# Kernel optimization log

Measured on AMD Instinct MI355X. Metric: run time of the kernel, lower is better.

## Reference

```python
import jax, jax.numpy as jnp
import numpy as np

DEPTH = 2
DIM = 64
INNER = 256  # hard-coded inner_dim in Attention
HEADS = 1
N = 4096
B = 2
EPS = 1e-5


def layernorm(x, g, b):
    m = jnp.mean(x, axis=-1, keepdims=True)
    v = jnp.var(x, axis=-1, keepdims=True)
    return (x - m) * jax.lax.rsqrt(v + EPS) * g + b


def setup_inputs() -> dict:
    key = jax.random.key(0)
    ks = jax.random.split(key, 16)
    embed = jax.random.normal(ks[0], (B, N, DIM), dtype=jnp.float32)
    A = jax.random.randint(ks[1], (1, HEADS, N, N), 0, 2).astype(jnp.float32)
    s = 0.02
    return {
        "embed": embed,
        "A": A,
        "g1": jnp.ones((DEPTH, DIM), jnp.float32),
        "b1": jnp.zeros((DEPTH, DIM), jnp.float32),
        "Wqkv": jax.random.normal(ks[2], (DEPTH, DIM, INNER * 3), jnp.float32) * s,
        "Wout": jax.random.normal(ks[3], (DEPTH, INNER, DIM), jnp.float32) * s,
        "bout": jnp.zeros((DEPTH, DIM), jnp.float32),
        "g2": jnp.ones((DEPTH, DIM), jnp.float32),
        "b2": jnp.zeros((DEPTH, DIM), jnp.float32),
        "W1": jax.random.normal(ks[4], (DEPTH, DIM, DIM), jnp.float32) * s,
        "bb1": jnp.zeros((DEPTH, DIM), jnp.float32),
        "W2": jax.random.normal(ks[5], (DEPTH, DIM, DIM), jnp.float32) * s,
        "bb2": jnp.zeros((DEPTH, DIM), jnp.float32),
        "gf": jnp.ones((DIM,), jnp.float32),
        "bf": jnp.zeros((DIM,), jnp.float32),
    }


def _encoder(embed, A, g1, b1, Wqkv, Wout, bout, g2, b2, W1, bb1, W2, bb2, gf, bf):
    b, n, dim = embed.shape
    scale = dim ** (-0.5)
    dh = INNER // HEADS
    x = embed
    attn = None
    dots_softmax = None
    diag = jnp.arange(n)
    for l in range(DEPTH):
        xn = layernorm(x, g1[l], b1[l])
        qkv = xn @ Wqkv[l]  # [b, n, 3*INNER]
        q, k, v = jnp.split(qkv, 3, axis=-1)
        # [b, n, INNER] -> [b, h, n, dh]
        q = q.reshape(b, n, HEADS, dh).transpose(0, 2, 1, 3)
        k = k.reshape(b, n, HEADS, dh).transpose(0, 2, 1, 3)
        v = v.reshape(b, n, HEADS, dh).transpose(0, 2, 1, 3)
        dots = jnp.einsum("bhid,bhjd->bhij", q, k) * scale
        dots_softmax = jax.nn.softmax(dots[0, 0], axis=-1)
        # adjacency mask, then only [0][0] kept; diagonal filled with literal 1.0;
        # the original does a cpu/numpy roundtrip with .detach() -> stop_gradient.
        e = jnp.where(A > 0, dots, jnp.float32(-9e15))[0, 0]  # [n, n]
        e = e.at[diag, diag].set(1.0)
        e = jax.lax.stop_gradient(e)
        attn = jax.nn.softmax(e, axis=-1)  # [n, n], shared across b, h
        out = jnp.einsum("ij,bhjd->bhid", attn, v)  # broadcast attn over b,h
        out = out.transpose(0, 2, 1, 3).reshape(b, n, INNER)
        out = out @ Wout[l] + bout[l]
        x = xn + out  # residual onto the NORMED input (as in original)
        xm = layernorm(x, g2[l], b2[l])
        mlp = jax.nn.gelu(xm @ W1[l] + bb1[l], approximate=False) @ W2[l] + bb2[l]
        x = xm + mlp
    x = layernorm(x, gf, bf)
    return x, attn.reshape(1, 1, n, n), dots_softmax


def reference(embed, A, g1, b1, Wqkv, Wout, bout, g2, b2, W1, bb1, W2, bb2, gf, bf):
    return _encoder(embed, A, g1, b1, Wqkv, Wout, bout, g2, b2, W1, bb1, W2, bb2, gf, bf)
```

## Files before the change

### kernel.cpp

```cpp
#include <hip/hip_runtime.h>
#include <hip/hip_bf16.h>
#include <math.h>

typedef __attribute__((ext_vector_type(8))) short short8;
typedef __attribute__((ext_vector_type(4))) float f32x4;

__device__ __forceinline__ unsigned short f2bf(float x) {
    __hip_bfloat16 b = __float2bfloat16(x);
    return *reinterpret_cast<unsigned short*>(&b);
}
__device__ __forceinline__ float gelu_exact(float x) {
    return 0.5f * x * (1.0f + erff(x * 0.70710678118654752f));
}

__global__ __launch_bounds__(256) void k_zero(float* __restrict__ p, long n)
{
    long i = (long)blockIdx.x * 256 + threadIdx.x;
    if (i < n) p[i] = 0.f;
}

__global__ __launch_bounds__(256) void k_layernorm(
    const float* __restrict__ x, const float* __restrict__ g,
    const float* __restrict__ b, float* __restrict__ out)
{
    int wave = threadIdx.x >> 6, lane = threadIdx.x & 63;
    long row = (long)blockIdx.x * 4 + wave;
    float v = x[row * 64 + lane];
    float s = v;
    #pragma unroll
    for (int o = 32; o; o >>= 1) s += __shfl_xor(s, o);
    float m = s * (1.0f / 64.0f);
    float d = v - m;
    float q = d * d;
    #pragma unroll
    for (int o = 32; o; o >>= 1) q += __shfl_xor(q, o);
    float rstd = rsqrtf(q * (1.0f / 64.0f) + 1e-5f);
    out[row * 64 + lane] = d * rstd * g[lane] + b[lane];
}

__global__ __launch_bounds__(256) void k_wfold(
    const float* __restrict__ Wqkv, const float* __restrict__ Wout,
    float* __restrict__ Wfold)
{
    int idx = blockIdx.x * 256 + threadIdx.x;
    int c = idx >> 6, d = idx & 63;
    float a = 0.f;
    for (int k = 0; k < 256; ++k)
        a += Wqkv[c * 768 + 512 + k] * Wout[k * 64 + d];
    Wfold[idx] = a;
}

__global__ __launch_bounds__(256) void k_maskpack(
    const float* __restrict__ Aadj, unsigned long long* __restrict__ mask)
{
    int row = blockIdx.x;
    int wave = threadIdx.x >> 6, lane = threadIdx.x & 63;
    for (int w = wave; w < 64; w += 4) {
        float a = Aadj[(long)row * 4096 + w * 64 + lane];
        unsigned long long m = __ballot(a > 0.f);
        if (lane == 0) mask[(long)row * 64 + w] = m;
    }
}

__global__ __launch_bounds__(256) void k_qk(
    const float* __restrict__ xn, const float* __restrict__ W,
    unsigned short* __restrict__ q, unsigned short* __restrict__ kmat)
{
    __shared__ float As[64][65];
    __shared__ float Ws[64][65];
    int tid = threadIdx.x;
    int m0 = blockIdx.x * 64, n0 = blockIdx.y * 64;
    #pragma unroll
    for (int it = 0; it < 16; ++it) {
        int idx = tid + it * 256;
        int r = idx >> 6, c = idx & 63;
        As[r][c] = xn[(long)(m0 + r) * 64 + c];
        Ws[r][c] = W[(long)r * 768 + n0 + c];
    }
    __syncthreads();
    int tx = tid & 15, ty = tid >> 4;
    float acc[4][4] = {};
    #pragma unroll
    for (int k = 0; k < 64; ++k) {
        float a[4], w[4];
        #pragma unroll
        for (int i = 0; i < 4; ++i) a[i] = As[ty * 4 + i][k];
        #pragma unroll
        for (int j = 0; j < 4; ++j) w[j] = Ws[k][tx * 4 + j];
        #pragma unroll
        for (int i = 0; i < 4; ++i)
            #pragma unroll
            for (int j = 0; j < 4; ++j) acc[i][j] += a[i] * w[j];
    }
    #pragma unroll
    for (int i = 0; i < 4; ++i) {
        long row = m0 + ty * 4 + i;
        #pragma unroll
        for (int j = 0; j < 4; ++j) {
            int col = n0 + tx * 4 + j;
            if (col < 256) q[row * 256 + col] = f2bf(acc[i][j]);
            else           kmat[row * 256 + (col - 256)] = f2bf(acc[i][j]);
        }
    }
}

__global__ __launch_bounds__(256) void k_xnw_t(
    const float* __restrict__ xn, const float* __restrict__ Wfold,
    unsigned short* __restrict__ vWT)
{
    __shared__ float As[64][65];
    __shared__ float Ws[64][65];
    int tid = threadIdx.x;
    int n0 = blockIdx.x * 64, b = blockIdx.y;
    #pragma unroll
    for (int it = 0; it < 16; ++it) {
        int idx = tid + it * 256;
        int r = idx >> 6, c = idx & 63;
        As[r][c] = xn[((long)b * 4096 + n0 + r) * 64 + c];
        Ws[r][c] = Wfold[r * 64 + c];
    }
    __syncthreads();
    int tx = tid & 15, ty = tid >> 4;
    float acc[4][4] = {};
    #pragma unroll
    for (int k = 0; k < 64; ++k) {
        float a[4], w[4];
        #pragma unroll
        for (int i = 0; i < 4; ++i) a[i] = As[ty * 4 + i][k];
        #pragma unroll
        for (int j = 0; j < 4; ++j) w[j] = Ws[k][tx * 4 + j];
        #pragma unroll
        for (int i = 0; i < 4; ++i)
            #pragma unroll
            for (int j = 0; j < 4; ++j) acc[i][j] += a[i] * w[j];
    }
    #pragma unroll
    for (int i = 0; i < 4; ++i)
        #pragma unroll
        for (int j = 0; j < 4; ++j)
            vWT[((long)b * 64 + tx * 4 + j) * 4096 + n0 + ty * 4 + i] = f2bf(acc[i][j]);
}

__global__ __launch_bounds__(256) void k_mfma_nt(
    const unsigned short* __restrict__ A, const unsigned short* __restrict__ B,
    float* __restrict__ C, int N, int K, float scale)
{
    __shared__ __align__(16) unsigned short As[128 * 64];
    __shared__ __align__(16) unsigned short Bs[128 * 64];
    int tid = threadIdx.x;
    int lane = tid & 63, wave = tid >> 6;
    long m0 = (long)blockIdx.x * 128, n0 = (long)blockIdx.y * 128;
    const unsigned short* Ag = A + m0 * K;
    const unsigned short* Bg = B + n0 * K;
    int wm = (wave & 1) * 64, wn = (wave >> 1) * 64;
    int fr = lane & 15, quad = lane >> 4;

    f32x4 acc[4][4];
    #pragma unroll
    for (int i = 0; i < 4; ++i)
        #pragma unroll
        for (int j = 0; j < 4; ++j) acc[i][j] = (f32x4){0.f, 0.f, 0.f, 0.f};

    for (int k0 = 0; k0 < K; k0 += 64) {
        #pragma unroll
        for (int it = 0; it < 4; ++it) {
            int c = tid + it * 256;
            int r = c >> 3, col = (c & 7) * 8;
            *(short8*)&As[c * 8] = *(const short8*)(Ag + (long)r * K + k0 + col);
            *(short8*)&Bs[c * 8] = *(const short8*)(Bg + (long)r * K + k0 + col);
        }
        __syncthreads();
        #pragma unroll
        for (int ks = 0; ks < 2; ++ks) {
            short8 af[4], bfr[4];
            #pragma unroll
            for (int i = 0; i < 4; ++i) {
                af[i]  = *(const short8*)&As[(wm + i * 16 + fr) * 64 + ks * 32 + quad * 8];
                bfr[i] = *(const short8*)&Bs[(wn + i * 16 + fr) * 64 + ks * 32 + quad * 8];
            }
            #pragma unroll
            for (int i = 0; i < 4; ++i)
                #pragma unroll
                for (int j = 0; j < 4; ++j)
                    acc[i][j] = __builtin_amdgcn_mfma_f32_16x16x32_bf16(
                        af[i], bfr[j], acc[i][j], 0, 0, 0);
        }
        __syncthreads();
    }
    #pragma unroll
    for (int i = 0; i < 4; ++i) {
        #pragma unroll
        for (int j = 0; j < 4; ++j) {
            long col = n0 + wn + j * 16 + fr;
            long rowb = m0 + wm + i * 16 + quad * 4;
            #pragma unroll
            for (int r = 0; r < 4; ++r)
                C[(rowb + r) * N + col] = acc[i][j][r] * scale;
        }
    }
}

__global__ __launch_bounds__(256) void k_mfma_splitk(
    const float* __restrict__ A, const unsigned short* __restrict__ B,
    float* __restrict__ C)
{
    __shared__ __align__(16) unsigned short As[128 * 64];
    __shared__ __align__(16) unsigned short Bs[128 * 64];
    const int K = 4096, N = 128;
    int tid = threadIdx.x;
    int lane = tid & 63, wave = tid >> 6;
    long m0 = (long)blockIdx.x * 128;
    int k0base = blockIdx.y * 512;
    const float* Ag = A + m0 * K;
    int wm = (wave & 1) * 64, wn = (wave >> 1) * 64;
    int fr = lane & 15, quad = lane >> 4;

    f32x4 acc[4][4];
    #pragma unroll
    for (int i = 0; i < 4; ++i)
        #pragma unroll
        for (int j = 0; j < 4; ++j) acc[i][j] = (f32x4){0.f, 0.f, 0.f, 0.f};

    for (int k0 = k0base; k0 < k0base + 512; k0 += 64) {
        #pragma unroll
        for (int it = 0; it < 4; ++it) {
            int c = tid + it * 256;
            int r = c >> 3, col = (c & 7) * 8;
            float4 f0 = *(const float4*)(Ag + (long)r * K + k0 + col);
            float4 f1 = *(const float4*)(Ag + (long)r * K + k0 + col + 4);
            short8 s;
            s[0] = (short)f2bf(f0.x); s[1] = (short)f2bf(f0.y);
            s[2] = (short)f2bf(f0.z); s[3] = (short)f2bf(f0.w);
            s[4] = (short)f2bf(f1.x); s[5] = (short)f2bf(f1.y);
            s[6] = (short)f2bf(f1.z); s[7] = (short)f2bf(f1.w);
            *(short8*)&As[c * 8] = s;
            *(short8*)&Bs[c * 8] = *(const short8*)(B + (long)r * K + k0 + col);
        }
        __syncthreads();
        #pragma unroll
        for (int ks = 0; ks < 2; ++ks) {
            short8 af[4], bfr[4];
            #pragma unroll
            for (int i = 0; i < 4; ++i) {
                af[i]  = *(const short8*)&As[(wm + i * 16 + fr) * 64 + ks * 32 + quad * 8];
                bfr[i] = *(const short8*)&Bs[(wn + i * 16 + fr) * 64 + ks * 32 + quad * 8];
            }
            #pragma unroll
            for (int i = 0; i < 4; ++i)
                #pragma unroll
                for (int j = 0; j < 4; ++j)
                    acc[i][j] = __builtin_amdgcn_mfma_f32_16x16x32_bf16(
                        af[i], bfr[j], acc[i][j], 0, 0, 0);
        }
        __syncthreads();
    }
    #pragma unroll
    for (int i = 0; i < 4; ++i) {
        #pragma unroll
        for (int j = 0; j < 4; ++j) {
            long col = wn + j * 16 + fr;
            long rowb = m0 + wm + i * 16 + quad * 4;
            #pragma unroll
            for (int r = 0; r < 4; ++r)
                atomicAdd(&C[(rowb + r) * N + col], acc[i][j][r]);
        }
    }
}

__device__ __forceinline__ float block_max(float v, float* red, int lane, int wave) {
    #pragma unroll
    for (int o = 32; o; o >>= 1) v = fmaxf(v, __shfl_xor(v, o));
    if (lane == 0) red[wave] = v;
    __syncthreads();
    v = fmaxf(fmaxf(red[0], red[1]), fmaxf(red[2], red[3]));
    __syncthreads();
    return v;
}
__device__ __forceinline__ float block_sum(float v, float* red, int lane, int wave) {
    #pragma unroll
    for (int o = 32; o; o >>= 1) v += __shfl_xor(v, o);
    if (lane == 0) red[wave] = v;
    __syncthreads();
    v = red[0] + red[1] + red[2] + red[3];
    __syncthreads();
    return v;
}

__global__ __launch_bounds__(256) void k_softmax_attn(
    float* __restrict__ dots, const float* __restrict__ Aadj,
    const unsigned long long* __restrict__ mask,
    float* __restrict__ attn_out, int write_ds)
{
    __shared__ float red[4];
    __shared__ unsigned long long msk[64];
    int row = blockIdx.x, tid = threadIdx.x;
    int lane = tid & 63, wave = tid >> 6;
    float* drow = dots + (long)row * 4096;
    if (mask) {
        if (tid < 64) msk[tid] = mask[(long)row * 64 + tid];
        __syncthreads();
    }
    float d[16], mv[16];
    float mmax = -1e30f, umax = -1e30f;
    #pragma unroll
    for (int i = 0; i < 16; ++i) {
        int j = tid + i * 256;
        float dv = drow[j];
        d[i] = dv;
        bool keep = mask ? ((msk[j >> 6] >> (j & 63)) & 1ull)
                         : (Aadj[(long)row * 4096 + j] > 0.f);
        float m = keep ? dv : -1e30f;
        if (j == row) m = 1.0f;
        mv[i] = m;
        mmax = fmaxf(mmax, m);
        umax = fmaxf(umax, dv);
    }
    float M1 = block_max(mmax, red, lane, wave);
    float s1 = 0.f;
    #pragma unroll
    for (int i = 0; i < 16; ++i) { float e = expf(mv[i] - M1); mv[i] = e; s1 += e; }
    s1 = block_sum(s1, red, lane, wave);
    float inv1 = 1.0f / s1;
    #pragma unroll
    for (int i = 0; i < 16; ++i)
        attn_out[(long)row * 4096 + tid + i * 256] = mv[i] * inv1;

    if (write_ds) {
        float M2 = block_max(umax, red, lane, wave);
        float s2 = 0.f;
        #pragma unroll
        for (int i = 0; i < 16; ++i) { float e = expf(d[i] - M2); d[i] = e; s2 += e; }
        s2 = block_sum(s2, red, lane, wave);
        float inv2 = 1.0f / s2;
        #pragma unroll
        for (int i = 0; i < 16; ++i)
            drow[tid + i * 256] = d[i] * inv2;
    }
}

__global__ __launch_bounds__(256) void k_avres(
    const float* __restrict__ xn, const float* __restrict__ avcat,
    const float* __restrict__ bout, float* __restrict__ x)
{
    int idx = blockIdx.x * 256 + threadIdx.x;
    int r = idx >> 6, c = idx & 63;
    int b = r >> 12, n = r & 4095;
    x[idx] = xn[idx] + avcat[(long)n * 128 + b * 64 + c] + bout[c];
}

__global__ __launch_bounds__(256) void k_gemm64(
    const float* __restrict__ A, const float* __restrict__ W,
    const float* __restrict__ bias, const float* __restrict__ res,
    float* __restrict__ out, int act)
{
    __shared__ float As[64][65];
    __shared__ float Ws[64][65];
    int tid = threadIdx.x;
    int m0 = blockIdx.x * 64;
    #pragma unroll
    for (int it = 0; it < 16; ++it) {
        int idx = tid + it * 256;
        int r = idx >> 6, c = idx & 63;
        As[r][c] = A[(long)(m0 + r) * 64 + c];
        Ws[r][c] = W[(long)r * 64 + c];
    }
    __syncthreads();
    int tx = tid & 15, ty = tid >> 4;
    float acc[4][4] = {};
    #pragma unroll
    for (int k = 0; k < 64; ++k) {
        float a[4], w[4];
        #pragma unroll
        for (int i = 0; i < 4; ++i) a[i] = As[ty * 4 + i][k];
        #pragma unroll
        for (int j = 0; j < 4; ++j) w[j] = Ws[k][tx * 4 + j];
        #pragma unroll
        for (int i = 0; i < 4; ++i)
            #pragma unroll
            for (int j = 0; j < 4; ++j) acc[i][j] += a[i] * w[j];
    }
    #pragma unroll
    for (int i = 0; i < 4; ++i) {
        long row = m0 + ty * 4 + i;
        #pragma unroll
        for (int j = 0; j < 4; ++j) {
            int col = tx * 4 + j;
            float v = acc[i][j] + bias[col];
            if (act) v = gelu_exact(v);
            if (res) v += res[row * 64 + col];
            out[row * 64 + col] = v;
        }
    }
}

extern "C" void kernel_launch(void* const* d_in, const int* in_sizes, int n_in,
                              void* d_out, int out_size, void* d_ws, size_t ws_size,
                              hipStream_t stream)
{
    const float* embed = (const float*)d_in[0];
    const float* Aadj  = (const float*)d_in[1];
    const float* g1    = (const float*)d_in[2];
    const float* b1    = (const float*)d_in[3];
    const float* Wqkv  = (const float*)d_in[4];
    const float* Wout  = (const float*)d_in[5];
    const float* bout  = (const float*)d_in[6];
    const float* g2    = (const float*)d_in[7];
    const float* b2    = (const float*)d_in[8];
    const float* W1    = (const float*)d_in[9];
    const float* bb1   = (const float*)d_in[10];
    const float* W2    = (const float*)d_in[11];
    const float* bb2   = (const float*)d_in[12];
    const float* gf    = (const float*)d_in[13];
    const float* bff   = (const float*)d_in[14];

    float* ox    = (float*)d_out;
    float* attnb = ox + 524288;
    float* dsb   = attnb + 16777216;

    if (ws_size < (10ull << 20)) {
        k_zero<<<133120, 256, 0, stream>>>(ox, 34078720l);
        return;
    }

    char* ws = (char*)d_ws;
    float*          x     = (float*)(ws + (0l << 20));
    float*          xn    = (float*)(ws + (2l << 20));
    float*          h     = (float*)(ws + (4l << 20));
    unsigned short* q     = (unsigned short*)(ws + (6l << 20));
    unsigned short* kmat  = (unsigned short*)(ws + (7l << 20));
    unsigned short* vwt   = (unsigned short*)(ws + (8l << 20));
    float*          Wfold = (float*)(ws + (9l << 20));
    unsigned long long* mask = (ws_size >= (12ull << 20))
        ? (unsigned long long*)(ws + (10l << 20)) : nullptr;

    if (mask) k_maskpack<<<4096, 256, 0, stream>>>(Aadj, mask);

    for (int l = 0; l < 2; ++l) {
        const float* Wq = Wqkv + (long)l * 64 * 768;
        k_layernorm<<<2048, 256, 0, stream>>>(l ? x : embed, g1 + 64 * l, b1 + 64 * l, xn);
        k_wfold<<<16, 256, 0, stream>>>(Wq, Wout + (long)l * 256 * 64, Wfold);
        k_qk<<<dim3(64, 8), 256, 0, stream>>>(xn, Wq, q, kmat);
        k_xnw_t<<<dim3(64, 2), 256, 0, stream>>>(xn, Wfold, vwt);
        k_mfma_nt<<<dim3(32, 32), 256, 0, stream>>>(q, kmat, dsb, 4096, 256, 0.125f);
        k_softmax_attn<<<4096, 256, 0, stream>>>(dsb, Aadj, mask, attnb, l == 1);
        k_zero<<<2048, 256, 0, stream>>>(ox, 524288l);
        k_mfma_splitk<<<dim3(32, 8), 256, 0, stream>>>(attnb, vwt, ox);
        k_avres<<<2048, 256, 0, stream>>>(xn, ox, bout + 64 * l, x);
        k_layernorm<<<2048, 256, 0, stream>>>(x, g2 + 64 * l, b2 + 64 * l, xn);
        k_gemm64<<<128, 256, 0, stream>>>(xn, W1 + (long)l * 4096, bb1 + 64 * l,
                                          nullptr, h, 1);
        k_gemm64<<<128, 256, 0, stream>>>(h, W2 + (long)l * 4096, bb2 + 64 * l,
                                          xn, x, 0);
    }
    k_layernorm<<<2048, 256, 0, stream>>>(x, gf, bff, ox);
}
```

Measured before the change: 520.3 us.

## Fuse tail MLP/layernorms, store dots and attn in bf16, batch weight folding

Several changes are combined. The residual, layernorm, both MLP GEMMs and the next or final layernorm are fused into one tail kernel. The Q/K and V-fold projections merge into one launch, and both layers' Wfold and the mask are built up front. When workspace allows, the dots and attention matrices are kept in bf16 scratch, and the fp32 attention and softmax outputs are written only for the final layer. This cuts launches and the large fp32 N×N traffic, at the cost of more bf16 rounding in layer 0's scores and branchy code paths that depend on workspace size.

New measurement: 536.4 us. 3.1% more time.

```diff
diff --git a/kernel.cpp b/kernel.cpp
--- a/kernel.cpp
+++ b/kernel.cpp
@@ -8,6 +8,9 @@
 __device__ __forceinline__ unsigned short f2bf(float x) {
     __hip_bfloat16 b = __float2bfloat16(x);
     return *reinterpret_cast<unsigned short*>(&b);
+}
+__device__ __forceinline__ float bfu2f(unsigned short u) {
+    union { unsigned u; float f; } c; c.u = ((unsigned)u) << 16; return c.f;
 }
 __device__ __forceinline__ float gelu_exact(float x) {
     return 0.5f * x * (1.0f + erff(x * 0.70710678118654752f));
@@ -38,15 +41,18 @@
     out[row * 64 + lane] = d * rstd * g[lane] + b[lane];
 }
 
-__global__ __launch_bounds__(256) void k_wfold(
+__global__ __launch_bounds__(256) void k_wfold2(
     const float* __restrict__ Wqkv, const float* __restrict__ Wout,
     float* __restrict__ Wfold)
 {
     int idx = blockIdx.x * 256 + threadIdx.x;
-    int c = idx >> 6, d = idx & 63;
+    int l = idx >> 12, rem = idx & 4095;
+    int c = rem >> 6, d = rem & 63;
+    const float* Wq = Wqkv + (long)l * 49152;
+    const float* Wo = Wout + (long)l * 16384;
     float a = 0.f;
     for (int k = 0; k < 256; ++k)
-        a += Wqkv[c * 768 + 512 + k] * Wout[k * 64 + d];
+        a += Wq[c * 768 + 512 + k] * Wo[k * 64 + d];
     Wfold[idx] = a;
 }
 
@@ -62,20 +68,26 @@
     }
 }
 
-__global__ __launch_bounds__(256) void k_qk(
+__global__ __launch_bounds__(256) void k_qkxnw(
     const float* __restrict__ xn, const float* __restrict__ W,
-    unsigned short* __restrict__ q, unsigned short* __restrict__ kmat)
+    const float* __restrict__ Wfold,
+    unsigned short* __restrict__ q, unsigned short* __restrict__ kmat,
+    unsigned short* __restrict__ vwt)
 {
     __shared__ float As[64][65];
     __shared__ float Ws[64][65];
     int tid = threadIdx.x;
-    int m0 = blockIdx.x * 64, n0 = blockIdx.y * 64;
+    int y = blockIdx.y;
+    int qk = (y < 8);
+    int m0, b = 0, n0;
+    if (qk) { m0 = blockIdx.x * 64; n0 = y * 64; }
+    else    { b = y - 8; m0 = b * 4096 + blockIdx.x * 64; n0 = 0; }
     #pragma unroll
     for (int it = 0; it < 16; ++it) {
         int idx = tid + it * 256;
         int r = idx >> 6, c = idx & 63;
         As[r][c] = xn[(long)(m0 + r) * 64 + c];
-        Ws[r][c] = W[(long)r * 768 + n0 + c];
+        Ws[r][c] = qk ? W[(long)r * 768 + n0 + c] : Wfold[r * 64 + c];
     }
     __syncthreads();
     int tx = tid & 15, ty = tid >> 4;
@@ -92,61 +104,34 @@
             #pragma unroll
             for (int j = 0; j < 4; ++j) acc[i][j] += a[i] * w[j];
     }
-    #pragma unroll
-    for (int i = 0; i < 4; ++i) {
-        long row = m0 + ty * 4 + i;
-        #pragma unroll
-        for (int j = 0; j < 4; ++j) {
-            int col = n0 + tx * 4 + j;
-            if (col < 256) q[row * 256 + col] = f2bf(acc[i][j]);
-            else           kmat[row * 256 + (col - 256)] = f2bf(acc[i][j]);
-        }
-    }
-}
-
-__global__ __launch_bounds__(256) void k_xnw_t(
-    const float* __restrict__ xn, const float* __restrict__ Wfold,
-    unsigned short* __restrict__ vWT)
-{
-    __shared__ float As[64][65];
-    __shared__ float Ws[64][65];
-    int tid = threadIdx.x;
-    int n0 = blockIdx.x * 64, b = blockIdx.y;
-    #pragma unroll
-    for (int it = 0; it < 16; ++it) {
-        int idx = tid + it * 256;
-        int r = idx >> 6, c = idx & 63;
-        As[r][c] = xn[((long)b * 4096 + n0 + r) * 64 + c];
-        Ws[r][c] = Wfold[r * 64 + c];
-    }
-    __syncthreads();
-    int tx = tid & 15, ty = tid >> 4;
-    float acc[4][4] = {};
-    #pragma unroll
-    for (int k = 0; k < 64; ++k) {
-        float a[4], w[4];
-        #pragma unroll
-        for (int i = 0; i < 4; ++i) a[i] = As[ty * 4 + i][k];
-        #pragma unroll
-        for (int j = 0; j < 4; ++j) w[j] = Ws[k][tx * 4 + j];
+    if (qk) {
+        #pragma unroll
+        for (int i = 0; i < 4; ++i) {
+            long row = m0 + ty * 4 + i;
+            #pragma unroll
+            for (int j = 0; j < 4; ++j) {
+                int col = n0 + tx * 4 + j;
+                if (col < 256) q[row * 256 + col] = f2bf(acc[i][j]);
+                else           kmat[row * 256 + (col - 256)] = f2bf(acc[i][j]);
+            }
+        }
+    } else {
+        int nb = blockIdx.x * 64;
         #pragma unroll
         for (int i = 0; i < 4; ++i)
             #pragma unroll
-            for (int j = 0; j < 4; ++j) acc[i][j] += a[i] * w[j];
-    }
-    #pragma unroll
-    for (int i = 0; i < 4; ++i)
-        #pragma unroll
-        for (int j = 0; j < 4; ++j)
-            vWT[((long)b * 64 + tx * 4 + j) * 4096 + n0 + ty * 4 + i] = f2bf(acc[i][j]);
-}
-
-__global__ __launch_bounds__(256) void k_mfma_nt(
+            for (int j = 0; j < 4; ++j)
+                vwt[((long)b * 64 + tx * 4 + j) * 4096 + nb + ty * 4 + i] = f2bf(acc[i][j]);
+    }
+}
+
+__global__ __launch_bounds__(256) void k_dots(
     const unsigned short* __restrict__ A, const unsigned short* __restrict__ B,
-    float* __restrict__ C, int N, int K, float scale)
+    unsigned short* __restrict__ Ch, float* __restrict__ Cf)
 {
     __shared__ __align__(16) unsigned short As[128 * 64];
     __shared__ __align__(16) unsigned short Bs[128 * 64];
+    const int K = 256;
     int tid = threadIdx.x;
     int lane = tid & 63, wave = tid >> 6;
     long m0 = (long)blockIdx.x * 128, n0 = (long)blockIdx.y * 128;
@@ -194,15 +179,18 @@
             long col = n0 + wn + j * 16 + fr;
             long rowb = m0 + wm + i * 16 + quad * 4;
             #pragma unroll
-            for (int r = 0; r < 4; ++r)
-                C[(rowb + r) * N + col] = acc[i][j][r] * scale;
-        }
-    }
-}
-
-__global__ __launch_bounds__(256) void k_mfma_splitk(
-    const float* __restrict__ A, const unsigned short* __restrict__ B,
-    float* __restrict__ C)
+            for (int r = 0; r < 4; ++r) {
+                float v = acc[i][j][r] * 0.125f;
+                if (Ch) Ch[(rowb + r) * 4096 + col] = f2bf(v);
+                else    Cf[(rowb + r) * 4096 + col] = v;
+            }
+        }
+    }
+}
+
+__global__ __launch_bounds__(256) void k_splitk(
+    const unsigned short* __restrict__ Ah, const float* __restrict__ Af,
+    const unsigned short* __restrict__ B, float* __restrict__ C)
 {
     __shared__ __align__(16) unsigned short As[128 * 64];
     __shared__ __align__(16) unsigned short Bs[128 * 64];
@@ -211,7 +199,6 @@
     int lane = tid & 63, wave = tid >> 6;
     long m0 = (long)blockIdx.x * 128;
     int k0base = blockIdx.y * 512;
-    const float* Ag = A + m0 * K;
     int wm = (wave & 1) * 64, wn = (wave >> 1) * 64;
     int fr = lane & 15, quad = lane >> 4;
 
@@ -226,14 +213,20 @@
         for (int it = 0; it < 4; ++it) {
             int c = tid + it * 256;
             int r = c >> 3, col = (c & 7) * 8;
-            float4 f0 = *(const float4*)(Ag + (long)r * K + k0 + col);
-            float4 f1 = *(const float4*)(Ag + (long)r * K + k0 + col + 4);
-            short8 s;
-            s[0] = (short)f2bf(f0.x); s[1] = (short)f2bf(f0.y);
-            s[2] = (short)f2bf(f0.z); s[3] = (short)f2bf(f0.w);
-            s[4] = (short)f2bf(f1.x); s[5] = (short)f2bf(f1.y);
-            s[6] = (short)f2bf(f1.z); s[7] = (short)f2bf(f1.w);
-            *(short8*)&As[c * 8] = s;
+            if (Ah) {
+                *(short8*)&As[c * 8] =
+                    *(const short8*)(Ah + (m0 + r) * (long)K + k0 + col);
+            } else {
+                const float* Ag = Af + m0 * K;
+                float4 f0 = *(const float4*)(Ag + (long)r * K + k0 + col);
+                float4 f1 = *(const float4*)(Ag + (long)r * K + k0 + col + 4);
+                short8 s;
+                s[0] = (short)f2bf(f0.x); s[1] = (short)f2bf(f0.y);
+                s[2] = (short)f2bf(f0.z); s[3] = (short)f2bf(f0.w);
+                s[4] = (short)f2bf(f1.x); s[5] = (short)f2bf(f1.y);
+                s[6] = (short)f2bf(f1.z); s[7] = (short)f2bf(f1.w);
+                *(short8*)&As[c * 8] = s;
+            }
             *(short8*)&Bs[c * 8] = *(const short8*)(B + (long)r * K + k0 + col);
         }
         __syncthreads();
@@ -286,31 +279,28 @@
     return v;
 }
 
-__global__ __launch_bounds__(256) void k_softmax_attn(
-    float* __restrict__ dots, const float* __restrict__ Aadj,
-    const unsigned long long* __restrict__ mask,
-    float* __restrict__ attn_out, int write_ds)
+__global__ __launch_bounds__(256) void k_softmax_bf(
+    const unsigned short* __restrict__ dots, const unsigned long long* __restrict__ mask,
+    unsigned short* __restrict__ attn_h, float* __restrict__ attn_f,
+    float* __restrict__ ds)
 {
     __shared__ float red[4];
-    __shared__ unsigned long long msk[64];
     int row = blockIdx.x, tid = threadIdx.x;
     int lane = tid & 63, wave = tid >> 6;
-    float* drow = dots + (long)row * 4096;
-    if (mask) {
-        if (tid < 64) msk[tid] = mask[(long)row * 64 + tid];
-        __syncthreads();
-    }
+    long base = (long)row * 4096 + tid * 16;
+    short8 v0 = *(const short8*)(dots + base);
+    short8 v1 = *(const short8*)(dots + base + 8);
+    unsigned long long mw = mask[(long)row * 64 + (tid >> 2)];
+    int mbase = (tid & 3) * 16;
+    int idiag = row - tid * 16;
     float d[16], mv[16];
     float mmax = -1e30f, umax = -1e30f;
     #pragma unroll
     for (int i = 0; i < 16; ++i) {
-        int j = tid + i * 256;
-        float dv = drow[j];
+        float dv = bfu2f((unsigned short)(i < 8 ? v0[i] : v1[i - 8]));
         d[i] = dv;
-        bool keep = mask ? ((msk[j >> 6] >> (j & 63)) & 1ull)
-                         : (Aadj[(long)row * 4096 + j] > 0.f);
-        float m = keep ? dv : -1e30f;
-        if (j == row) m = 1.0f;
+        float m = ((mw >> (mbase + i)) & 1ull) ? dv : -1e30f;
+        if (i == idiag) m = 1.0f;
         mv[i] = m;
         mmax = fmaxf(mmax, m);
         umax = fmaxf(umax, dv);
@@ -321,11 +311,22 @@
     for (int i = 0; i < 16; ++i) { float e = expf(mv[i] - M1); mv[i] = e; s1 += e; }
     s1 = block_sum(s1, red, lane, wave);
     float inv1 = 1.0f / s1;
-    #pragma unroll
-    for (int i = 0; i < 16; ++i)
-        attn_out[(long)row * 4096 + tid + i * 256] = mv[i] * inv1;
-
-    if (write_ds) {
+    short8 o0, o1;
+    #pragma unroll
+    for (int i = 0; i < 16; ++i) {
+        float p = mv[i] * inv1;
+        mv[i] = p;
+        if (i < 8) o0[i] = (short)f2bf(p); else o1[i - 8] = (short)f2bf(p);
+    }
+    *(short8*)(attn_h + base) = o0;
+    *(short8*)(attn_h + base + 8) = o1;
+    if (attn_f) {
+        #pragma unroll
+        for (int i = 0; i < 4; ++i)
+            *(float4*)(attn_f + base + i * 4) =
+                (float4){mv[i * 4], mv[i * 4 + 1], mv[i * 4 + 2], mv[i * 4 + 3]};
+    }
+    if (ds) {
         float M2 = block_max(umax, red, lane, wave);
         float s2 = 0.f;
         #pragma unroll
@@ -333,63 +334,172 @@
         s2 = block_sum(s2, red, lane, wave);
         float inv2 = 1.0f / s2;
         #pragma unroll
-        for (int i = 0; i < 16; ++i)
-            drow[tid + i * 256] = d[i] * inv2;
-    }
-}
-
-__global__ __launch_bounds__(256) void k_avres(
+        for (int i = 0; i < 4; ++i)
+            *(float4*)(ds + base + i * 4) =
+                (float4){d[i * 4] * inv2, d[i * 4 + 1] * inv2,
+                         d[i * 4 + 2] * inv2, d[i * 4 + 3] * inv2};
+    }
+}
+
+__global__ __launch_bounds__(256) void k_softmax_f32(
+    float* __restrict__ dots, const unsigned long long* __restrict__ mask,
+    float* __restrict__ attn_f)
+{
+    __shared__ float red[4];
+    int row = blockIdx.x, tid = threadIdx.x;
+    int lane = tid & 63, wave = tid >> 6;
+    long base = (long)row * 4096 + tid * 16;
+    float d[16], mv[16];
+    #pragma unroll
+    for (int i = 0; i < 4; ++i) {
+        float4 f = *(const float4*)(dots + base + i * 4);
+        d[i * 4] = f.x; d[i * 4 + 1] = f.y; d[i * 4 + 2] = f.z; d[i * 4 + 3] = f.w;
+    }
+    unsigned long long mw = mask[(long)row * 64 + (tid >> 2)];
+    int mbase = (tid & 3) * 16;
+    int idiag = row - tid * 16;
+    float mmax = -1e30f, umax = -1e30f;
+    #pragma unroll
+    for (int i = 0; i < 16; ++i) {
+        float m = ((mw >> (mbase + i)) & 1ull) ? d[i] : -1e30f;
+        if (i == idiag) m = 1.0f;
+        mv[i] = m;
+        mmax = fmaxf(mmax, m);
+        umax = fmaxf(umax, d[i]);
+    }
+    float M1 = block_max(mmax, red, lane, wave);
+    float s1 = 0.f;
+    #pragma unroll
+    for (int i = 0; i < 16; ++i) { float e = expf(mv[i] - M1); mv[i] = e; s1 += e; }
+    s1 = block_sum(s1, red, lane, wave);
+    float inv1 = 1.0f / s1;
+    #pragma unroll
+    for (int i = 0; i < 4; ++i)
+        *(float4*)(attn_f + base + i * 4) =
+            (float4){mv[i * 4] * inv1, mv[i * 4 + 1] * inv1,
+                     mv[i * 4 + 2] * inv1, mv[i * 4 + 3] * inv1};
+    float M2 = block_max(umax, red, lane, wave);
+    float s2 = 0.f;
+    #pragma unroll
+    for (int i = 0; i < 16; ++i) { float e = expf(d[i] - M2); d[i] = e; s2 += e; }
+    s2 = block_sum(s2, red, lane, wave);
+    float inv2 = 1.0f / s2;
+    #pragma unroll
+    for (int i = 0; i < 4; ++i)
+        *(float4*)(dots + base + i * 4) =
+            (float4){d[i * 4] * inv2, d[i * 4 + 1] * inv2,
+                     d[i * 4 + 2] * inv2, d[i * 4 + 3] * inv2};
+}
+
+__global__ __launch_bounds__(256) void k_tail(
     const float* __restrict__ xn, const float* __restrict__ avcat,
-    const float* __restrict__ bout, float* __restrict__ x)
-{
-    int idx = blockIdx.x * 256 + threadIdx.x;
-    int r = idx >> 6, c = idx & 63;
-    int b = r >> 12, n = r & 4095;
-    x[idx] = xn[idx] + avcat[(long)n * 128 + b * 64 + c] + bout[c];
-}
-
-__global__ __launch_bounds__(256) void k_gemm64(
-    const float* __restrict__ A, const float* __restrict__ W,
-    const float* __restrict__ bias, const float* __restrict__ res,
-    float* __restrict__ out, int act)
-{
-    __shared__ float As[64][65];
-    __shared__ float Ws[64][65];
+    const float* __restrict__ bout,
+    const float* __restrict__ g2, const float* __restrict__ b2,
+    const float* __restrict__ W1, const float* __restrict__ bb1,
+    const float* __restrict__ W2, const float* __restrict__ bb2,
+    const float* __restrict__ gn, const float* __restrict__ bn,
+    float* __restrict__ out)
+{
+    __shared__ float X[64][65], XM[64][65], H[64][65], WS[64][65];
     int tid = threadIdx.x;
     int m0 = blockIdx.x * 64;
+    int wv = tid >> 6, ln = tid & 63;
     #pragma unroll
     for (int it = 0; it < 16; ++it) {
         int idx = tid + it * 256;
         int r = idx >> 6, c = idx & 63;
-        As[r][c] = A[(long)(m0 + r) * 64 + c];
-        Ws[r][c] = W[(long)r * 64 + c];
+        int gr = m0 + r;
+        X[r][c] = xn[(long)gr * 64 + c]
+                + avcat[(long)(gr & 4095) * 128 + (gr >> 12) * 64 + c]
+                + bout[c];
+    }
+    __syncthreads();
+    #pragma unroll
+    for (int rr = 0; rr < 16; ++rr) {
+        int r = wv * 16 + rr;
+        float v = X[r][ln];
+        float s = v;
+        #pragma unroll
+        for (int o = 32; o; o >>= 1) s += __shfl_xor(s, o);
+        float m = s * (1.0f / 64.0f);
+        float dd = v - m;
+        float q = dd * dd;
+        #pragma unroll
+        for (int o = 32; o; o >>= 1) q += __shfl_xor(q, o);
+        float rstd = rsqrtf(q * (1.0f / 64.0f) + 1e-5f);
+        XM[r][ln] = dd * rstd * g2[ln] + b2[ln];
+    }
+    __syncthreads();
+    #pragma unroll
+    for (int it = 0; it < 16; ++it) {
+        int idx = tid + it * 256;
+        WS[idx >> 6][idx & 63] = W1[idx];
     }
     __syncthreads();
     int tx = tid & 15, ty = tid >> 4;
-    float acc[4][4] = {};
-    #pragma unroll
-    for (int k = 0; k < 64; ++k) {
-        float a[4], w[4];
-        #pragma unroll
-        for (int i = 0; i < 4; ++i) a[i] = As[ty * 4 + i][k];
-        #pragma unroll
-        for (int j = 0; j < 4; ++j) w[j] = Ws[k][tx * 4 + j];
+    {
+        float acc[4][4] = {};
+        #pragma unroll
+        for (int k = 0; k < 64; ++k) {
+            float a[4], w[4];
+            #pragma unroll
+            for (int i = 0; i < 4; ++i) a[i] = XM[ty * 4 + i][k];
+            #pragma unroll
+            for (int j = 0; j < 4; ++j) w[j] = WS[k][tx * 4 + j];
+            #pragma unroll
+            for (int i = 0; i < 4; ++i)
+                #pragma unroll
+                for (int j = 0; j < 4; ++j) acc[i][j] += a[i] * w[j];
+        }
         #pragma unroll
         for (int i = 0; i < 4; ++i)
             #pragma unroll
-            for (int j = 0; j < 4; ++j) acc[i][j] += a[i] * w[j];
-    }
-    #pragma unroll
-    for (int i = 0; i < 4; ++i) {
-        long row = m0 + ty * 4 + i;
-        #pragma unroll
-        for (int j = 0; j < 4; ++j) {
-            int col = tx * 4 + j;
-            float v = acc[i][j] + bias[col];
-            if (act) v = gelu_exact(v);
-            if (res) v += res[row * 64 + col];
-            out[row * 64 + col] = v;
-        }
+            for (int j = 0; j < 4; ++j)
+                H[ty * 4 + i][tx * 4 + j] = gelu_exact(acc[i][j] + bb1[tx * 4 + j]);
+    }
+    __syncthreads();
+    #pragma unroll
+    for (int it = 0; it < 16; ++it) {
+        int idx = tid + it * 256;
+        WS[idx >> 6][idx & 63] = W2[idx];
+    }
+    __syncthreads();
+    {
+        float acc[4][4] = {};
+        #pragma unroll
+        for (int k = 0; k < 64; ++k) {
+            float a[4], w[4];
+            #pragma unroll
+            for (int i = 0; i < 4; ++i) a[i] = H[ty * 4 + i][k];
+            #pragma unroll
+            for (int j = 0; j < 4; ++j) w[j] = WS[k][tx * 4 + j];
+            #pragma unroll
+            for (int i = 0; i < 4; ++i)
+                #pragma unroll
+                for (int j = 0; j < 4; ++j) acc[i][j] += a[i] * w[j];
+        }
+        #pragma unroll
+        for (int i = 0; i < 4; ++i)
+            #pragma unroll
+            for (int j = 0; j < 4; ++j)
+                X[ty * 4 + i][tx * 4 + j] =
+                    XM[ty * 4 + i][tx * 4 + j] + acc[i][j] + bb2[tx * 4 + j];
+    }
+    __syncthreads();
+    #pragma unroll
+    for (int rr = 0; rr < 16; ++rr) {
+        int r = wv * 16 + rr;
+        float v = X[r][ln];
+        float s = v;
+        #pragma unroll
+        for (int o = 32; o; o >>= 1) s += __shfl_xor(s, o);
+        float m = s * (1.0f / 64.0f);
+        float dd = v - m;
+        float q = dd * dd;
+        #pragma unroll
+        for (int o = 32; o; o >>= 1) q += __shfl_xor(q, o);
+        float rstd = rsqrtf(q * (1.0f / 64.0f) + 1e-5f);
+        out[(long)(m0 + r) * 64 + ln] = dd * rstd * gn[ln] + bn[ln];
     }
 }
 
@@ -423,34 +533,49 @@
     }
 
     char* ws = (char*)d_ws;
-    float*          x     = (float*)(ws + (0l << 20));
-    float*          xn    = (float*)(ws + (2l << 20));
-    float*          h     = (float*)(ws + (4l << 20));
-    unsigned short* q     = (unsigned short*)(ws + (6l << 20));
-    unsigned short* kmat  = (unsigned short*)(ws + (7l << 20));
-    unsigned short* vwt   = (unsigned short*)(ws + (8l << 20));
-    float*          Wfold = (float*)(ws + (9l << 20));
-    unsigned long long* mask = (ws_size >= (12ull << 20))
-        ? (unsigned long long*)(ws + (10l << 20)) : nullptr;
-
-    if (mask) k_maskpack<<<4096, 256, 0, stream>>>(Aadj, mask);
+    float*          xn    = (float*)(ws + (0l << 20));
+    float*          avcat = (float*)(ws + (2l << 20));
+    unsigned short* q     = (unsigned short*)(ws + (4l << 20));
+    unsigned short* kmat  = (unsigned short*)(ws + (5l << 20));
+    unsigned short* vwt   = (unsigned short*)(ws + (6l << 20));
+    float*          Wfold = (float*)(ws + (7l << 20));
+    unsigned long long* mask = (unsigned long long*)(ws + (7l << 20) + 32768);
+    unsigned short* wsbuf = (unsigned short*)(ws + (10l << 20));
+    bool rich = ws_size >= (42ull << 20);
+
+    k_layernorm<<<2048, 256, 0, stream>>>(embed, g1, b1, xn);
+    k_wfold2<<<32, 256, 0, stream>>>(Wqkv, Wout, Wfold);
+    k_maskpack<<<4096, 256, 0, stream>>>(Aadj, mask);
 
     for (int l = 0; l < 2; ++l) {
-        const float* Wq = Wqkv + (long)l * 64 * 768;
-        k_layernorm<<<2048, 256, 0, stream>>>(l ? x : embed, g1 + 64 * l, b1 + 64 * l, xn);
-        k_wfold<<<16, 256, 0, stream>>>(Wq, Wout + (long)l * 256 * 64, Wfold);
-        k_qk<<<dim3(64, 8), 256, 0, stream>>>(xn, Wq, q, kmat);
-        k_xnw_t<<<dim3(64, 2), 256, 0, stream>>>(xn, Wfold, vwt);
-        k_mfma_nt<<<dim3(32, 32), 256, 0, stream>>>(q, kmat, dsb, 4096, 256, 0.125f);
-        k_softmax_attn<<<4096, 256, 0, stream>>>(dsb, Aadj, mask, attnb, l == 1);
-        k_zero<<<2048, 256, 0, stream>>>(ox, 524288l);
-        k_mfma_splitk<<<dim3(32, 8), 256, 0, stream>>>(attnb, vwt, ox);
-        k_avres<<<2048, 256, 0, stream>>>(xn, ox, bout + 64 * l, x);
-        k_layernorm<<<2048, 256, 0, stream>>>(x, g2 + 64 * l, b2 + 64 * l, xn);
-        k_gemm64<<<128, 256, 0, stream>>>(xn, W1 + (long)l * 4096, bb1 + 64 * l,
-                                          nullptr, h, 1);
-        k_gemm64<<<128, 256, 0, stream>>>(h, W2 + (long)l * 4096, bb2 + 64 * l,
-                                          xn, x, 0);
-    }
-    k_layernorm<<<2048, 256, 0, stream>>>(x, gf, bff, ox);
-}
+        k_qkxnw<<<dim3(64, 10), 256, 0, stream>>>(xn, Wqkv + (long)l * 49152,
+                                                  Wfold + l * 4096, q, kmat, vwt);
+        if (rich) {
+            k_dots<<<dim3(32, 32), 256, 0, stream>>>(q, kmat, wsbuf, nullptr);
+            k_softmax_bf<<<4096, 256, 0, stream>>>(wsbuf, mask, wsbuf,
+                                                   l ? attnb : nullptr,
+                                                   l ? dsb : nullptr);
+            k_zero<<<2048, 256, 0, stream>>>(avcat, 524288l);
+            k_splitk<<<dim3(32, 8), 256, 0, stream>>>(wsbuf, nullptr, vwt, avcat);
+        } else if (l == 0) {
+            unsigned short* dots_h = (unsigned short*)dsb;
+            unsigned short* attn_h = (unsigned short*)attnb;
+            k_dots<<<dim3(32, 32), 256, 0, stream>>>(q, kmat, dots_h, nullptr);
+            k_softmax_bf<<<4096, 256, 0, stream>>>(dots_h, mask, attn_h,
+                                                   nullptr, nullptr);
+            k_zero<<<2048, 256, 0, stream>>>(avcat, 524288l);
+            k_splitk<<<dim3(32, 8), 256, 0, stream>>>(attn_h, nullptr, vwt, avcat);
+        } else {
+            k_dots<<<dim3(32, 32), 256, 0, stream>>>(q, kmat, nullptr, dsb);
+            k_softmax_f32<<<4096, 256, 0, stream>>>(dsb, mask, attnb);
+            k_zero<<<2048, 256, 0, stream>>>(avcat, 524288l);
+            k_splitk<<<dim3(32, 8), 256, 0, stream>>>(nullptr, attnb, vwt, avcat);
+        }
+        k_tail<<<128, 256, 0, stream>>>(xn, avcat, bout + 64 * l,
+                                        g2 + 64 * l, b2 + 64 * l,
+                                        W1 + (long)l * 4096, bb1 + 64 * l,
+                                        W2 + (long)l * 4096, bb2 + 64 * l,
+                                        l ? gf : g1 + 64, l ? bff : b1 + 64,
+                                        l ? ox : xn);
+    }
+}
```
